# Optimization experiments

Measured on AMD Instinct MI355X. Metric: run time of the kernel, lower is better.

## Reference

```python
import jax, jax.numpy as jnp
import numpy as np
from functools import partial

C = 96
D_STATE = 16
D_CONV = 4
EXPAND = 2
D_INNER = EXPAND * C
DT_RANK = (C + 15) // 16  # ceil(96/16) = 6
EPS = 1e-6


def _ln_cf(x, w, b):
    # channels_first LayerNorm over axis=1 of [B,C,D,H,W]
    u = jnp.mean(x, axis=1, keepdims=True)
    s = jnp.mean((x - u) ** 2, axis=1, keepdims=True)
    xn = (x - u) / jnp.sqrt(s + EPS)
    return w[None, :, None, None, None] * xn + b[None, :, None, None, None]


def _ln_last(x, w, b):
    u = jnp.mean(x, axis=-1, keepdims=True)
    s = jnp.mean((x - u) ** 2, axis=-1, keepdims=True)
    return (x - u) / jnp.sqrt(s + 1e-5) * w + b


def _mamba(x, Win, conv_w, conv_b, Wx, Wdt, bdt, A_log, Dp, Wout):
    # x: [B, L, C]
    B, L, _ = x.shape
    xz = jnp.einsum('blc,ec->ble', x, Win)           # [B,L,2*di]
    xin, z = xz[..., :D_INNER], xz[..., D_INNER:]
    # depthwise causal conv along L
    xt = jnp.transpose(xin, (0, 2, 1))               # [B,di,L]
    xt = jnp.pad(xt, ((0, 0), (0, 0), (D_CONV - 1, 0)))
    xc = jax.lax.conv_general_dilated(
        xt, conv_w[:, None, :], window_strides=(1,), padding='VALID',
        feature_group_count=D_INNER, dimension_numbers=('NCH', 'OIH', 'NCH'))
    xc = jax.nn.silu(xc + conv_b[None, :, None])
    xc = jnp.transpose(xc, (0, 2, 1))                # [B,L,di]
    x_dbl = jnp.einsum('bld,ed->ble', xc, Wx)        # [B,L,dt_rank+2*ds]
    dt_r = x_dbl[..., :DT_RANK]
    Bm = x_dbl[..., DT_RANK:DT_RANK + D_STATE]       # [B,L,ds]
    Cm = x_dbl[..., DT_RANK + D_STATE:]              # [B,L,ds]
    dt = jax.nn.softplus(jnp.einsum('blr,dr->bld', dt_r, Wdt) + bdt)
    A = -jnp.exp(A_log)                              # [di,ds]
    dA = jnp.exp(dt[..., None] * A)                  # [B,L,di,ds]
    dBx = (dt * xc)[..., None] * Bm[:, :, None, :]   # [B,L,di,ds]

    def comb(e1, e2):
        a1, b1 = e1
        a2, b2 = e2
        return a1 * a2, a2 * b1 + b2

    _, h = jax.lax.associative_scan(comb, (dA, dBx), axis=1)
    y = jnp.einsum('blds,bls->bld', h, Cm) + xc * Dp
    y = y * jax.nn.silu(z)
    return jnp.einsum('bld,cd->blc', y, Wout)


def setup_inputs() -> dict:
    key = jax.random.key(0)
    ks = jax.random.split(key, 16)
    g = lambda k, sh: jax.random.normal(k, sh, dtype=jnp.float32) * 0.02
    inp = {
        'x': jax.random.normal(ks[0], (2, C, 20, 20, 20), dtype=jnp.float32),
        'ln_w': jnp.ones((C,), jnp.float32), 'ln_b': jnp.zeros((C,), jnp.float32),
        'mln_w': jnp.ones((C,), jnp.float32), 'mln_b': jnp.zeros((C,), jnp.float32),
        'Win': g(ks[1], (2 * D_INNER, C)),
        'conv_w': g(ks[2], (D_INNER, D_CONV)), 'conv_b': jnp.zeros((D_INNER,), jnp.float32),
        'Wx': g(ks[3], (DT_RANK + 2 * D_STATE, D_INNER)),
        'Wdt': g(ks[4], (D_INNER, DT_RANK)), 'bdt': g(ks[5], (D_INNER,)),
        'A_log': jnp.log(jnp.broadcast_to(jnp.arange(1, D_STATE + 1, dtype=jnp.float32), (D_INNER, D_STATE))),
        'Dp': jnp.ones((D_INNER,), jnp.float32),
        'Wout': g(ks[6], (C, D_INNER)),
        'proj_w': g(ks[7], (C, 3 * C)), 'proj_b': jnp.zeros((C,), jnp.float32),
        'fc1_w': g(ks[8], (4 * C, C)), 'fc1_b': jnp.zeros((4 * C,), jnp.float32),
        'fc2_w': g(ks[9], (C, 4 * C)), 'fc2_b': jnp.zeros((C,), jnp.float32),
    }
    return inp


def reference(x, ln_w, ln_b, mln_w, mln_b, Win, conv_w, conv_b, Wx, Wdt, bdt,
              A_log, Dp, Wout, proj_w, proj_b, fc1_w, fc1_b, fc2_w, fc2_b):
    B, Cc, Dd, Hh, Ww = x.shape
    L = Dd * Hh * Ww
    x1 = _ln_cf(x, ln_w, ln_b)
    # three directional flattenings (cube, so reshape shapes match)
    outs = []
    for perm in ((0, 1, 2, 3, 4), (0, 1, 3, 4, 2), (0, 1, 4, 2, 3)):
        xp = jnp.transpose(x1, perm)                     # [B,C,a,b,c]
        xf = jnp.transpose(xp.reshape(B, Cc, L), (0, 2, 1))  # [B,L,C]
        xf = _ln_last(xf, mln_w, mln_b)
        y = _mamba(xf, Win, conv_w, conv_b, Wx, Wdt, bdt, A_log, Dp, Wout)
        outs.append(jnp.transpose(y, (0, 2, 1)).reshape(B, Cc, Dd, Hh, Ww))
    cat = jnp.concatenate(outs, axis=1)                  # [B,3C,D,H,W]
    out1 = jnp.einsum('oc,bcdhw->bodhw', proj_w, cat) + proj_b[None, :, None, None, None]
    out_res = x + out1
    h = _ln_cf(out_res, ln_w, ln_b)
    h = jnp.einsum('oc,bcdhw->bodhw', fc1_w, h) + fc1_b[None, :, None, None, None]
    h = jax.nn.gelu(h, approximate=False)
    h = jnp.einsum('oc,bcdhw->bodhw', fc2_w, h) + fc2_b[None, :, None, None, None]
    return h + out_res
```

## Files before the change

### kernel.cpp

```cpp
#include <hip/hip_runtime.h>
#include <math.h>

#define S   8000
#define BB  2
#define CC  96
#define DI  192
#define NS  16
#define RK  6
#define GG  6
#define NC  200
#define LC  40
#define ND  38

typedef __attribute__((ext_vector_type(8))) short bf16x8;
typedef __attribute__((ext_vector_type(4))) float f32x4;
typedef __attribute__((ext_vector_type(2))) float f32x2;

__device__ __forceinline__ int pos_from_l(int dir, int l) {
  if (dir == 0) return l;
  int a  = l / 400;
  int r  = l - a * 400;
  int bq = r / 20;
  int cq = r - bq * 20;
  if (dir == 1) return cq * 400 + a * 20 + bq;
  return bq * 400 + cq * 20 + a;
}

__device__ __forceinline__ float silu(float z) {
  return z / (1.f + __expf(-z));
}

__device__ __forceinline__ unsigned short f2bf(float x) {
  unsigned int u = __float_as_uint(x);
  u += 0x7FFFu + ((u >> 16) & 1u);
  return (unsigned short)(u >> 16);
}
__device__ __forceinline__ float bf2f(unsigned short h) {
  return __uint_as_float((unsigned int)h << 16);
}

__device__ __forceinline__ float pair_sum(float y) {
  return y + __int_as_float(__builtin_amdgcn_update_dpp(
      0, __float_as_int(y), 0xB1, 0xF, 0xF, true));
}
__device__ __forceinline__ float quad_sum(float x) {
  x += __int_as_float(__builtin_amdgcn_update_dpp(0, __float_as_int(x), 0xB1, 0xF, 0xF, true));
  x += __int_as_float(__builtin_amdgcn_update_dpp(0, __float_as_int(x), 0x4E, 0xF, 0xF, true));
  return x;
}

template <int ACT, bool DOUBLE, bool OUTBF16>
__global__ __launch_bounds__(256) void k_lnmfma(const float* __restrict__ Xsrc,
    const float* __restrict__ lnw, const float* __restrict__ lnb,
    const float* __restrict__ mlnw, const float* __restrict__ mlnb,
    const float* __restrict__ Bw, const float* __restrict__ bias,
    void* __restrict__ Cout, int M, int N) {
  __shared__ float Xf[64][97];
  __shared__ unsigned short Al[64][104];
  __shared__ unsigned short Bl[96][104];
  int tid = threadIdx.x;
  int m0 = blockIdx.x * 64, n0 = blockIdx.y * 96;
  int b = m0 / S, pos0 = m0 - b * S;
  for (int idx = tid; idx < 64 * 96; idx += 256) {
    int row = idx & 63, c = idx >> 6;
    Xf[row][c] = Xsrc[((size_t)b * CC + c) * S + pos0 + row];
  }
  for (int idx = tid; idx < 96 * 24; idx += 256) {
    int bn = idx / 24, kq = idx - bn * 24;
    int n = n0 + bn;
    float4 v = make_float4(0.f, 0.f, 0.f, 0.f);
    if (n < N) v = *(const float4*)&Bw[(size_t)n * 96 + kq * 4];
    unsigned short* dst = &Bl[bn][kq * 4];
    dst[0] = f2bf(v.x); dst[1] = f2bf(v.y);
    dst[2] = f2bf(v.z); dst[3] = f2bf(v.w);
  }
  __syncthreads();
  {
    int row = tid >> 2, part = tid & 3;
    const float* xr = &Xf[row][part * 24];
    float s1 = 0.f, s2 = 0.f;
#pragma unroll
    for (int i = 0; i < 24; ++i) { float v = xr[i]; s1 += v; s2 += v * v; }
    s1 = quad_sum(s1); s2 = quad_sum(s2);
    float u = s1 * (1.f / 96.f);
    float var = s2 * (1.f / 96.f) - u * u;
    float rstd = rsqrtf(var + 1e-6f);
    if (DOUBLE) {
      float t1 = 0.f, t2 = 0.f;
#pragma unroll
      for (int i = 0; i < 24; ++i) {
        int c = part * 24 + i;
        float y1 = fmaf(lnw[c], (xr[i] - u) * rstd, lnb[c]);
        t1 += y1; t2 += y1 * y1;
      }
      t1 = quad_sum(t1); t2 = quad_sum(t2);
      float u2 = t1 * (1.f / 96.f);
      float var2 = t2 * (1.f / 96.f) - u2 * u2;
      float rstd2 = rsqrtf(var2 + 1e-5f);
#pragma unroll
      for (int i = 0; i < 24; ++i) {
        int c = part * 24 + i;
        float y1 = fmaf(lnw[c], (xr[i] - u) * rstd, lnb[c]);
        Al[row][c] = f2bf(fmaf(mlnw[c], (y1 - u2) * rstd2, mlnb[c]));
      }
    } else {
#pragma unroll
      for (int i = 0; i < 24; ++i) {
        int c = part * 24 + i;
        Al[row][c] = f2bf(fmaf(lnw[c], (xr[i] - u) * rstd, lnb[c]));
      }
    }
  }
  __syncthreads();
  int wid = tid >> 6, lane = tid & 63;
  int wr = wid >> 1, wc = wid & 1;
  int l16 = lane & 15, lk = (lane >> 4) * 8;
  f32x4 acc[2][3];
#pragma unroll
  for (int i = 0; i < 2; ++i)
#pragma unroll
    for (int j = 0; j < 3; ++j) acc[i][j] = (f32x4){0.f, 0.f, 0.f, 0.f};
#pragma unroll
  for (int kc = 0; kc < 96; kc += 32) {
    bf16x8 af[2], bfr[3];
#pragma unroll
    for (int i = 0; i < 2; ++i)
      af[i] = *(const bf16x8*)&Al[wr * 32 + i * 16 + l16][kc + lk];
#pragma unroll
    for (int j = 0; j < 3; ++j)
      bfr[j] = *(const bf16x8*)&Bl[wc * 48 + j * 16 + l16][kc + lk];
#pragma unroll
    for (int i = 0; i < 2; ++i)
#pragma unroll
      for (int j = 0; j < 3; ++j)
        acc[i][j] = __builtin_amdgcn_mfma_f32_16x16x32_bf16(
            af[i], bfr[j], acc[i][j], 0, 0, 0);
  }
#pragma unroll
  for (int i = 0; i < 2; ++i) {
#pragma unroll
    for (int j = 0; j < 3; ++j) {
#pragma unroll
      for (int v = 0; v < 4; ++v) {
        int m = m0 + wr * 32 + i * 16 + (lane >> 4) * 4 + v;
        int n = n0 + wc * 48 + j * 16 + l16;
        if (n < N) {
          float val = acc[i][j][v];
          val += bias ? bias[n] : 0.f;
          if (ACT == 1) val = 0.5f * val * (1.f + erff(val * 0.70710678118654752f));
          if (OUTBF16) ((unsigned short*)Cout)[(size_t)m * N + n] = f2bf(val);
          else         ((float*)Cout)[(size_t)m * N + n] = val;
        }
      }
    }
  }
}

#define BKP 40
template <int ACT, bool BIAS, bool RESID, bool OUT_BCS, bool GATEA, bool ABF16>
__global__ __launch_bounds__(256) void k_mfma(const void* __restrict__ Ap,
    const float* __restrict__ Bw, const float* __restrict__ bias,
    const float* __restrict__ resid, const float* __restrict__ XZg,
    float* __restrict__ Cmat, int M, int N, int K) {
  __shared__ unsigned short Al[64][BKP];
  __shared__ unsigned short Bl[96][BKP];
  int tid = threadIdx.x;
  int m0 = blockIdx.x * 64, n0 = blockIdx.y * 96;
  int wid = tid >> 6, lane = tid & 63;
  int wr = wid >> 1, wc = wid & 1;
  int l16 = lane & 15, lk = (lane >> 4) * 8;
  f32x4 acc[2][3];
#pragma unroll
  for (int i = 0; i < 2; ++i)
#pragma unroll
    for (int j = 0; j < 3; ++j) acc[i][j] = (f32x4){0.f, 0.f, 0.f, 0.f};

  for (int kk = 0; kk < K; kk += 32) {
    if (ABF16) {
      int row = tid >> 2, kq = tid & 3;
      int m = m0 + row;
      const unsigned short* As = (const unsigned short*)Ap;
      uint4 v = *(const uint4*)&As[(size_t)m * K + kk + kq * 8];
      if (GATEA) {
        unsigned short* pv = (unsigned short*)&v;
        int bb = m / S, ll = m - bb * S;
        int j = kk + kq * 8;
        int dir = j / DI; int e0 = j - dir * DI;
        int p = pos_from_l(dir, ll);
        const float4 z1 = *(const float4*)&XZg[((size_t)bb * S + p) * 384 + DI + e0];
        const float4 z2 = *(const float4*)&XZg[((size_t)bb * S + p) * 384 + DI + e0 + 4];
        pv[0] = f2bf(bf2f(pv[0]) * silu(z1.x));
        pv[1] = f2bf(bf2f(pv[1]) * silu(z1.y));
        pv[2] = f2bf(bf2f(pv[2]) * silu(z1.z));
        pv[3] = f2bf(bf2f(pv[3]) * silu(z1.w));
        pv[4] = f2bf(bf2f(pv[4]) * silu(z2.x));
        pv[5] = f2bf(bf2f(pv[5]) * silu(z2.y));
        pv[6] = f2bf(bf2f(pv[6]) * silu(z2.z));
        pv[7] = f2bf(bf2f(pv[7]) * silu(z2.w));
      }
      *(uint4*)&Al[row][kq * 8] = v;
    } else {
#pragma unroll
      for (int i = 0; i < 2; ++i) {
        int idx = tid + i * 256;
        int row = idx >> 3, kq = idx & 7;
        int m = m0 + row;
        const float* Af = (const float*)Ap;
        float4 v = *(const float4*)&Af[(size_t)m * K + kk + kq * 4];
        unsigned short* dst = &Al[row][kq * 4];
        dst[0] = f2bf(v.x); dst[1] = f2bf(v.y);
        dst[2] = f2bf(v.z); dst[3] = f2bf(v.w);
      }
    }
#pragma unroll
    for (int i = 0; i < 3; ++i) {
      int idx = tid + i * 256;
      int bn = idx >> 3, kq = idx & 7;
      int n = n0 + bn;
      float4 v = make_float4(0.f, 0.f, 0.f, 0.f);
      if (n < N) v = *(const float4*)&Bw[(size_t)n * K + kk + kq * 4];
      unsigned short* dst = &Bl[bn][kq * 4];
      dst[0] = f2bf(v.x); dst[1] = f2bf(v.y);
      dst[2] = f2bf(v.z); dst[3] = f2bf(v.w);
    }
    __syncthreads();
    bf16x8 af[2], bfr[3];
#pragma unroll
    for (int i = 0; i < 2; ++i)
      af[i] = *(const bf16x8*)&Al[wr * 32 + i * 16 + l16][lk];
#pragma unroll
    for (int j = 0; j < 3; ++j)
      bfr[j] = *(const bf16x8*)&Bl[wc * 48 + j * 16 + l16][lk];
#pragma unroll
    for (int i = 0; i < 2; ++i)
#pragma unroll
      for (int j = 0; j < 3; ++j)
        acc[i][j] = __builtin_amdgcn_mfma_f32_16x16x32_bf16(
            af[i], bfr[j], acc[i][j], 0, 0, 0);
    __syncthreads();
  }
#pragma unroll
  for (int i = 0; i < 2; ++i) {
#pragma unroll
    for (int j = 0; j < 3; ++j) {
#pragma unroll
      for (int v = 0; v < 4; ++v) {
        int m = m0 + wr * 32 + i * 16 + (lane >> 4) * 4 + v;
        int n = n0 + wc * 48 + j * 16 + l16;
        if (n < N) {
          float val = acc[i][j][v];
          if (BIAS) val += bias[n];
          if (ACT == 1) val = 0.5f * val * (1.f + erff(val * 0.70710678118654752f));
          if (RESID || OUT_BCS) {
            int bb = m / S, pp = m - bb * S;
            size_t oidx = ((size_t)bb * CC + n) * S + pp;
            if (RESID) val += resid[oidx];
            if (OUT_BCS) { Cmat[oidx] = val; continue; }
          }
          Cmat[(size_t)m * N + n] = val;
        }
      }
    }
  }
}

__global__ __launch_bounds__(256) void k_conv(const float* __restrict__ XZ,
    const float* __restrict__ cw, const float* __restrict__ cb,
    float* __restrict__ xc) {
  int t = blockIdx.x * blockDim.x + threadIdx.x;
  if (t >= GG * S * 48) return;
  int q = t % 48; int gl = t / 48; int l = gl % S; int g = gl / S;
  int e0 = q * 4;
  int b = g / 3, dir = g - (g / 3) * 3;
  float cwv[4][4];
#pragma unroll
  for (int i = 0; i < 4; ++i)
    *(float4*)cwv[i] = *(const float4*)&cw[(e0 + i) * 4];
  float4 acc = *(const float4*)&cb[e0];
#pragma unroll
  for (int k = 0; k < 4; ++k) {
    int ls = l + k - 3;
    if (ls >= 0) {
      int p = pos_from_l(dir, ls);
      const float4 xz = *(const float4*)&XZ[((size_t)b * S + p) * 384 + e0];
      acc.x = fmaf(cwv[0][k], xz.x, acc.x);
      acc.y = fmaf(cwv[1][k], xz.y, acc.y);
      acc.z = fmaf(cwv[2][k], xz.z, acc.z);
      acc.w = fmaf(cwv[3][k], xz.w, acc.w);
    }
  }
  acc.x *= 1.f / (1.f + __expf(-acc.x));
  acc.y *= 1.f / (1.f + __expf(-acc.y));
  acc.z *= 1.f / (1.f + __expf(-acc.z));
  acc.w *= 1.f / (1.f + __expf(-acc.w));
  *(float4*)&xc[(size_t)gl * DI + e0] = acc;
}

__device__ __forceinline__ void stage_bc(float (*sBC)[40],
    const float* __restrict__ xdbl, int g, int c, int tid) {
  const float* src = xdbl + ((size_t)g * S + c * LC) * ND;
  for (int i = tid; i < LC * ND; i += 192) {
    int row = i / ND, col = i - row * ND;
    int dst = (col < RK) ? col : col + 2;
    sBC[row][dst] = src[(size_t)row * ND + col];
  }
}

#define DT_COMMON(l)                                                     \
  float a = bde;                                                         \
  {                                                                      \
    float4 r0 = *(const float4*)&sBC[l][0];                              \
    float2 r1 = *(const float2*)&sBC[l][4];                              \
    a = fmaf(wdt[0], r0.x, a); a = fmaf(wdt[1], r0.y, a);                \
    a = fmaf(wdt[2], r0.z, a); a = fmaf(wdt[3], r0.w, a);                \
    a = fmaf(wdt[4], r1.x, a); a = fmaf(wdt[5], r1.y, a);                \
  }                                                                      \
  float d = fmaxf(a, 0.f) + __logf(1.f + __expf(-fabsf(a)));

__global__ __launch_bounds__(192) void k_scanA(const float* __restrict__ xc,
    const float* __restrict__ xdbl, const float* __restrict__ Wdt,
    const float* __restrict__ bdt, const float* __restrict__ A_log,
    float* __restrict__ PA, float* __restrict__ EA) {
  __shared__ float sBC[LC][40];
  int c = blockIdx.x, g = blockIdx.y;
  int tid = threadIdx.x;
  int e = blockIdx.z * 96 + (tid >> 1);
  int hf = tid & 1;
  stage_bc(sBC, xdbl, g, c, tid);
  float wdt[RK];
#pragma unroll
  for (int r = 0; r < RK; ++r) wdt[r] = Wdt[e * RK + r];
  float bde = bdt[e];
  float base = -__expf(A_log[e * NS]);
  bool fast = true;
#pragma unroll
  for (int s = 1; s < NS; ++s) {
    float aes = -__expf(A_log[e * NS + s]);
    fast = fast && (fabsf(aes / base - (float)(s + 1)) < 1e-3f);
  }
  f32x2 h2[4];
#pragma unroll
  for (int k = 0; k < 4; ++k) h2[k] = (f32x2){0.f, 0.f};
  float T = 0.f;
  const float* xptr = xc + ((size_t)g * S + c * LC) * DI + e;
  __syncthreads();
  if (fast) {
    for (int l0 = 0; l0 < LC; l0 += 8) {
      float xb[8];
#pragma unroll
      for (int j = 0; j < 8; ++j) xb[j] = xptr[(size_t)(l0 + j) * DI];
#pragma unroll
      for (int j = 0; j < 8; ++j) {
        int l = l0 + j;
        DT_COMMON(l)
        T += d;
        float w = d * xb[j];
        float r = __expf(d * base);
        float r2 = r * r, r4 = r2 * r2, r8 = r4 * r4;
        float f = hf ? r8 * r : r;
        f32x2 m0 = {f, f * r};
        f32x2 r2v = {r2, r2};
        f32x2 r4v = {r4, r4};
        f32x2 m1 = m0 * r2v, m2 = m0 * r4v, m3 = m1 * r4v;
        f32x2 wv = {w, w};
        float4 Ba = *(const float4*)&sBC[l][8 + hf * 8];
        float4 Bb = *(const float4*)&sBC[l][12 + hf * 8];
        h2[0] = m0 * h2[0] + wv * (f32x2){Ba.x, Ba.y};
        h2[1] = m1 * h2[1] + wv * (f32x2){Ba.z, Ba.w};
        h2[2] = m2 * h2[2] + wv * (f32x2){Bb.x, Bb.y};
        h2[3] = m3 * h2[3] + wv * (f32x2){Bb.z, Bb.w};
      }
    }
  } else {
    float Aes[8];
#pragma unroll
    for (int k = 0; k < 8; ++k) Aes[k] = -__expf(A_log[e * NS + hf * 8 + k]);
#pragma unroll 1
    for (int l = 0; l < LC; ++l) {
      DT_COMMON(l)
      T += d;
      float w = d * xptr[(size_t)l * DI];
#pragma unroll
      for (int k = 0; k < 8; ++k) {
        float q = __expf(d * Aes[k]);
        h2[k >> 1][k & 1] = fmaf(q, h2[k >> 1][k & 1], w * sBC[l][8 + hf * 8 + k]);
      }
    }
  }
  float* pp = PA + (((size_t)g * NC + c) * DI + e) * NS + hf * 8;
  float* ep = EA + (((size_t)g * NC + c) * DI + e) * NS + hf * 8;
  float po[8];
  if (fast) {
    float r = __expf(base * T);
    float r2 = r * r, r4 = r2 * r2, r8 = r4 * r4;
    float f = hf ? r8 * r : r;
    po[0] = f; po[1] = f * r; po[2] = f * r2; po[3] = po[1] * r2;
    po[4] = f * r4; po[5] = po[1] * r4; po[6] = po[2] * r4; po[7] = po[3] * r4;
  } else {
#pragma unroll
    for (int k = 0; k < 8; ++k)
      po[k] = __expf(-__expf(A_log[e * NS + hf * 8 + k]) * T);
  }
  *(float4*)&pp[0] = make_float4(po[0], po[1], po[2], po[3]);
  *(float4*)&pp[4] = make_float4(po[4], po[5], po[6], po[7]);
  *(float4*)&ep[0] = make_float4(h2[0][0], h2[0][1], h2[1][0], h2[1][1]);
  *(float4*)&ep[4] = make_float4(h2[2][0], h2[2][1], h2[3][0], h2[3][1]);
}

__global__ __launch_bounds__(256) void k_scanB(const float* PA,
    const float* EA, float* Hin) {
  int idx = blockIdx.x * blockDim.x + threadIdx.x;
  if (idx >= GG * DI * NS) return;
  int g = idx / (DI * NS); int es = idx - g * (DI * NS);
  size_t stride = (size_t)DI * NS;
  size_t b0 = (size_t)g * NC * stride + es;
  float h = 0.f;
  for (int c0 = 0; c0 < NC; c0 += 8) {
    float p8[8], e8[8];
#pragma unroll
    for (int j = 0; j < 8; ++j) {
      size_t ix = b0 + (size_t)(c0 + j) * stride;
      p8[j] = PA[ix]; e8[j] = EA[ix];
    }
#pragma unroll
    for (int j = 0; j < 8; ++j) {
      size_t ix = b0 + (size_t)(c0 + j) * stride;
      Hin[ix] = h;
      h = fmaf(p8[j], h, e8[j]);
    }
  }
}

__global__ __launch_bounds__(192) void k_scanC(const float* __restrict__ xc,
    const float* __restrict__ xdbl, const float* __restrict__ Wdt,
    const float* __restrict__ bdt, const float* __restrict__ A_log,
    const float* __restrict__ Hin, const float* __restrict__ Dp,
    unsigned short* __restrict__ ygb) {
  __shared__ float sBC[LC][40];
  int c = blockIdx.x, g = blockIdx.y;
  int tid = threadIdx.x;
  int e = blockIdx.z * 96 + (tid >> 1);
  int hf = tid & 1;
  const float* hp = Hin + (((size_t)g * NC + c) * DI + e) * NS + hf * 8;
  float4 h0 = *(const float4*)(hp + 0);
  float4 h1v = *(const float4*)(hp + 4);
  stage_bc(sBC, xdbl, g, c, tid);
  float wdt[RK];
#pragma unroll
  for (int r = 0; r < RK; ++r) wdt[r] = Wdt[e * RK + r];
  float bde = bdt[e];
  float dpe = Dp[e];
  float base = -__expf(A_log[e * NS]);
  bool fast = true;
#pragma unroll
  for (int s = 1; s < NS; ++s) {
    float aes = -__expf(A_log[e * NS + s]);
    fast = fast && (fabsf(aes / base - (float)(s + 1)) < 1e-3f);
  }
  f32x2 h2[4] = {{h0.x, h0.y}, {h0.z, h0.w}, {h1v.x, h1v.y}, {h1v.z, h1v.w}};
  const float* xptr = xc + ((size_t)g * S + c * LC) * DI + e;
  int b = g / 3, dir = g - (g / 3) * 3;
  unsigned short* yo = ygb + ((size_t)b * S + c * LC) * 576 + dir * DI + e;
  __syncthreads();
  if (fast) {
    for (int l0 = 0; l0 < LC; l0 += 8) {
      float xb[8];
#pragma unroll
      for (int j = 0; j < 8; ++j) xb[j] = xptr[(size_t)(l0 + j) * DI];
#pragma unroll
      for (int j = 0; j < 8; ++j) {
        int l = l0 + j;
        DT_COMMON(l)
        float xv = xb[j];
        float w = d * xv;
        float r = __expf(d * base);
        float r2 = r * r, r4 = r2 * r2, r8 = r4 * r4;
        float f = hf ? r8 * r : r;
        f32x2 m0 = {f, f * r};
        f32x2 r2v = {r2, r2};
        f32x2 r4v = {r4, r4};
        f32x2 m1 = m0 * r2v, m2 = m0 * r4v, m3 = m1 * r4v;
        f32x2 wv = {w, w};
        float4 Ba = *(const float4*)&sBC[l][8 + hf * 8];
        float4 Bb = *(const float4*)&sBC[l][12 + hf * 8];
        float4 Ca = *(const float4*)&sBC[l][24 + hf * 8];
        float4 Cb = *(const float4*)&sBC[l][28 + hf * 8];
        f32x2 yacc = {hf ? 0.f : xv * dpe, 0.f};
        h2[0] = m0 * h2[0] + wv * (f32x2){Ba.x, Ba.y};
        yacc += h2[0] * (f32x2){Ca.x, Ca.y};
        h2[1] = m1 * h2[1] + wv * (f32x2){Ba.z, Ba.w};
        yacc += h2[1] * (f32x2){Ca.z, Ca.w};
        h2[2] = m2 * h2[2] + wv * (f32x2){Bb.x, Bb.y};
        yacc += h2[2] * (f32x2){Cb.x, Cb.y};
        h2[3] = m3 * h2[3] + wv * (f32x2){Bb.z, Bb.w};
        yacc += h2[3] * (f32x2){Cb.z, Cb.w};
        float ysum = pair_sum(yacc[0] + yacc[1]);
        if (!hf) yo[(size_t)l * 576] = f2bf(ysum);
      }
    }
  } else {
    float Aes[8];
#pragma unroll
    for (int k = 0; k < 8; ++k) Aes[k] = -__expf(A_log[e * NS + hf * 8 + k]);
#pragma unroll 1
    for (int l = 0; l < LC; ++l) {
      DT_COMMON(l)
      float xv = xptr[(size_t)l * DI];
      float w = d * xv;
      float y = hf ? 0.f : xv * dpe;
#pragma unroll
      for (int k = 0; k < 8; ++k) {
        float q = __expf(d * Aes[k]);
        float hk = fmaf(q, h2[k >> 1][k & 1], w * sBC[l][8 + hf * 8 + k]);
        h2[k >> 1][k & 1] = hk;
        y = fmaf(hk, sBC[l][24 + hf * 8 + k], y);
      }
      float ysum = pair_sum(y);
      if (!hf) yo[(size_t)l * 576] = f2bf(ysum);
    }
  }
}

__global__ __launch_bounds__(256) void k_foldW(const float* __restrict__ proj_w,
    const float* __restrict__ Wout, float* __restrict__ Mcat) {
  int t = blockIdx.x * blockDim.x + threadIdx.x;
  if (t >= CC * 576) return;
  int o = t / 576; int j = t - o * 576; int dir = j / DI; int e = j - dir * DI;
  float a = 0.f;
  for (int c2 = 0; c2 < CC; ++c2)
    a = fmaf(proj_w[o * 288 + dir * CC + c2], Wout[c2 * DI + e], a);
  Mcat[t] = a;
}

extern "C" void kernel_launch(void* const* d_in, const int* in_sizes, int n_in,
                              void* d_out, int out_size, void* d_ws, size_t ws_size,
                              hipStream_t stream) {
  const float* x      = (const float*)d_in[0];
  const float* ln_w   = (const float*)d_in[1];
  const float* ln_b   = (const float*)d_in[2];
  const float* mln_w  = (const float*)d_in[3];
  const float* mln_b  = (const float*)d_in[4];
  const float* Win    = (const float*)d_in[5];
  const float* conv_w = (const float*)d_in[6];
  const float* conv_b = (const float*)d_in[7];
  const float* Wx     = (const float*)d_in[8];
  const float* Wdt    = (const float*)d_in[9];
  const float* bdt    = (const float*)d_in[10];
  const float* A_log  = (const float*)d_in[11];
  const float* Dp     = (const float*)d_in[12];
  const float* Wout   = (const float*)d_in[13];
  const float* proj_w = (const float*)d_in[14];
  const float* proj_b = (const float*)d_in[15];
  const float* fc1_w  = (const float*)d_in[16];
  const float* fc1_b  = (const float*)d_in[17];
  const float* fc2_w  = (const float*)d_in[18];
  const float* fc2_b  = (const float*)d_in[19];

  float* ws = (float*)d_ws;
  size_t off = 0;
  float* ores = ws + off; off += (size_t)BB * S * CC;
  float* XZ   = ws + off; off += (size_t)BB * S * 384;
  float* xc   = ws + off; off += (size_t)GG * S * DI;
  float* xdbl = ws + off; off += (size_t)GG * S * ND;
  float* PA   = ws + off; off += (size_t)GG * NC * DI * NS;
  float* EA   = ws + off; off += (size_t)GG * NC * DI * NS;
  float* yg   = ws + off; off += (size_t)BB * S * 576;
  float* Mcat = ws + off; off += (size_t)CC * 576;
  if (ws_size < off * sizeof(float)) return;
  float* Hin  = PA;
  unsigned short* ygb = (unsigned short*)yg;
  unsigned short* h1  = (unsigned short*)XZ;

  k_lnmfma<0, true, false><<<dim3(BB * S / 64, 4), 256, 0, stream>>>(
      x, ln_w, ln_b, mln_w, mln_b, Win, nullptr, XZ, BB * S, 384);
  k_conv<<<(GG * S * 48 + 255) / 256, 256, 0, stream>>>(XZ, conv_w, conv_b, xc);
  k_mfma<0, false, false, false, false, false>
      <<<dim3(GG * S / 64, 1), 256, 0, stream>>>(
      xc, Wx, nullptr, nullptr, nullptr, xdbl, GG * S, ND, DI);
  k_scanA<<<dim3(NC, GG, 2), 192, 0, stream>>>(xc, xdbl, Wdt, bdt, A_log, PA, EA);
  k_scanB<<<(GG * DI * NS + 255) / 256, 256, 0, stream>>>(PA, EA, Hin);
  k_scanC<<<dim3(NC, GG, 2), 192, 0, stream>>>(xc, xdbl, Wdt, bdt, A_log, Hin, Dp, ygb);
  k_foldW<<<(CC * 576 + 255) / 256, 256, 0, stream>>>(proj_w, Wout, Mcat);
  k_mfma<0, true, true, true, true, true>
      <<<dim3(BB * S / 64, 1), 256, 0, stream>>>(
      ygb, Mcat, proj_b, x, XZ, ores, BB * S, CC, 576);
  k_lnmfma<1, false, true><<<dim3(BB * S / 64, 4), 256, 0, stream>>>(
      ores, ln_w, ln_b, nullptr, nullptr, fc1_w, fc1_b, h1, BB * S, 384);
  k_mfma<0, true, true, true, false, true>
      <<<dim3(BB * S / 64, 1), 256, 0, stream>>>(
      h1, fc2_w, fc2_b, ores, nullptr, (float*)d_out, BB * S, CC, 384);
}
```

Baseline: 267.9 us.

## Store conv output in bf16 and precompute dt and decay in fp16

The conv kernel now writes xc as bf16, and the x_proj GEMM reads it as bf16. A new k_dtr kernel computes softplus(dt) and exp(dt*A0) once per element into fp16 buffers, so scanA and scanC no longer recompute them. Both scans stage only the B/C columns in shared memory. The aim is to cut memory traffic and duplicated transcendental work in the two scan passes, at the cost of an extra kernel launch, an extra round trip through memory, and reduced precision for dt and the decay factor.

```diff
diff --git a/kernel.cpp b/kernel.cpp
--- a/kernel.cpp
+++ b/kernel.cpp
@@ -1,4 +1,5 @@
 #include <hip/hip_runtime.h>
+#include <hip/hip_fp16.h>
 #include <math.h>
 
 #define S   8000
@@ -266,7 +267,7 @@
 
 __global__ __launch_bounds__(256) void k_conv(const float* __restrict__ XZ,
     const float* __restrict__ cw, const float* __restrict__ cb,
-    float* __restrict__ xc) {
+    unsigned short* __restrict__ xcb) {
   int t = blockIdx.x * blockDim.x + threadIdx.x;
   if (t >= GG * S * 48) return;
   int q = t % 48; int gl = t / 48; int l = gl % S; int g = gl / S;
@@ -289,48 +290,58 @@
       acc.w = fmaf(cwv[3][k], xz.w, acc.w);
     }
   }
-  acc.x *= 1.f / (1.f + __expf(-acc.x));
-  acc.y *= 1.f / (1.f + __expf(-acc.y));
-  acc.z *= 1.f / (1.f + __expf(-acc.z));
-  acc.w *= 1.f / (1.f + __expf(-acc.w));
-  *(float4*)&xc[(size_t)gl * DI + e0] = acc;
-}
-
-__device__ __forceinline__ void stage_bc(float (*sBC)[40],
+  unsigned short o[4];
+  o[0] = f2bf(acc.x * (1.f / (1.f + __expf(-acc.x))));
+  o[1] = f2bf(acc.y * (1.f / (1.f + __expf(-acc.y))));
+  o[2] = f2bf(acc.z * (1.f / (1.f + __expf(-acc.z))));
+  o[3] = f2bf(acc.w * (1.f / (1.f + __expf(-acc.w))));
+  *(uint2*)&xcb[(size_t)gl * DI + e0] = *(uint2*)o;
+}
+
+__global__ __launch_bounds__(256) void k_dtr(const float* __restrict__ xdbl,
+    const float* __restrict__ Wdt, const float* __restrict__ bdt,
+    const float* __restrict__ A_log, __half* __restrict__ dtb,
+    __half* __restrict__ rb) {
+  int t = blockIdx.x * blockDim.x + threadIdx.x;
+  if (t >= GG * S * DI) return;
+  int e = t % DI; int row = t / DI;
+  const float* xr = xdbl + (size_t)row * ND;
+  float a = bdt[e];
+#pragma unroll
+  for (int r = 0; r < RK; ++r) a = fmaf(Wdt[e * RK + r], xr[r], a);
+  float d = fmaxf(a, 0.f) + __logf(1.f + __expf(-fabsf(a)));
+  float base = -__expf(A_log[e * NS]);
+  dtb[t] = __float2half(d);
+  rb[t] = __float2half(__expf(d * base));
+}
+
+__device__ __forceinline__ void stage_b16(float (*sB)[16],
     const float* __restrict__ xdbl, int g, int c, int tid) {
-  const float* src = xdbl + ((size_t)g * S + c * LC) * ND;
-  for (int i = tid; i < LC * ND; i += 192) {
-    int row = i / ND, col = i - row * ND;
-    int dst = (col < RK) ? col : col + 2;
-    sBC[row][dst] = src[(size_t)row * ND + col];
-  }
-}
-
-#define DT_COMMON(l)                                                     \
-  float a = bde;                                                         \
-  {                                                                      \
-    float4 r0 = *(const float4*)&sBC[l][0];                              \
-    float2 r1 = *(const float2*)&sBC[l][4];                              \
-    a = fmaf(wdt[0], r0.x, a); a = fmaf(wdt[1], r0.y, a);                \
-    a = fmaf(wdt[2], r0.z, a); a = fmaf(wdt[3], r0.w, a);                \
-    a = fmaf(wdt[4], r1.x, a); a = fmaf(wdt[5], r1.y, a);                \
-  }                                                                      \
-  float d = fmaxf(a, 0.f) + __logf(1.f + __expf(-fabsf(a)));
-
-__global__ __launch_bounds__(192) void k_scanA(const float* __restrict__ xc,
-    const float* __restrict__ xdbl, const float* __restrict__ Wdt,
-    const float* __restrict__ bdt, const float* __restrict__ A_log,
+  const float* src = xdbl + ((size_t)g * S + c * LC) * ND + RK;
+  for (int i = tid; i < LC * 16; i += 192) {
+    int row = i >> 4, col = i & 15;
+    sB[row][col] = src[(size_t)row * ND + col];
+  }
+}
+__device__ __forceinline__ void stage_bc32(float (*sBC)[32],
+    const float* __restrict__ xdbl, int g, int c, int tid) {
+  const float* src = xdbl + ((size_t)g * S + c * LC) * ND + RK;
+  for (int i = tid; i < LC * 32; i += 192) {
+    int row = i >> 5, col = i & 31;
+    sBC[row][col] = src[(size_t)row * ND + col];
+  }
+}
+
+__global__ __launch_bounds__(192) void k_scanA(const unsigned short* __restrict__ xcb,
+    const __half* __restrict__ dtb, const __half* __restrict__ rbuf,
+    const float* __restrict__ xdbl, const float* __restrict__ A_log,
     float* __restrict__ PA, float* __restrict__ EA) {
-  __shared__ float sBC[LC][40];
+  __shared__ float sB[LC][16];
   int c = blockIdx.x, g = blockIdx.y;
   int tid = threadIdx.x;
   int e = blockIdx.z * 96 + (tid >> 1);
   int hf = tid & 1;
-  stage_bc(sBC, xdbl, g, c, tid);
-  float wdt[RK];
-#pragma unroll
-  for (int r = 0; r < RK; ++r) wdt[r] = Wdt[e * RK + r];
-  float bde = bdt[e];
+  stage_b16(sB, xdbl, g, c, tid);
   float base = -__expf(A_log[e * NS]);
   bool fast = true;
 #pragma unroll
@@ -342,29 +353,36 @@
 #pragma unroll
   for (int k = 0; k < 4; ++k) h2[k] = (f32x2){0.f, 0.f};
   float T = 0.f;
-  const float* xptr = xc + ((size_t)g * S + c * LC) * DI + e;
+  size_t sbase = ((size_t)g * S + c * LC) * DI + e;
+  const unsigned short* xp = xcb + sbase;
+  const __half* dp = dtb + sbase;
+  const __half* rp = rbuf + sbase;
   __syncthreads();
   if (fast) {
     for (int l0 = 0; l0 < LC; l0 += 8) {
-      float xb[8];
-#pragma unroll
-      for (int j = 0; j < 8; ++j) xb[j] = xptr[(size_t)(l0 + j) * DI];
+      float xb[8], db[8], rv[8];
+#pragma unroll
+      for (int j = 0; j < 8; ++j) {
+        xb[j] = bf2f(xp[(size_t)(l0 + j) * DI]);
+        db[j] = __half2float(dp[(size_t)(l0 + j) * DI]);
+        rv[j] = __half2float(rp[(size_t)(l0 + j) * DI]);
+      }
 #pragma unroll
       for (int j = 0; j < 8; ++j) {
         int l = l0 + j;
-        DT_COMMON(l)
+        float d = db[j];
         T += d;
         float w = d * xb[j];
-        float r = __expf(d * base);
+        float r = rv[j];
         float r2 = r * r, r4 = r2 * r2, r8 = r4 * r4;
         float f = hf ? r8 * r : r;
         f32x2 m0 = {f, f * r};
-        f32x2 r2v = {r2, r2};
-        f32x2 r4v = {r4, r4};
-        f32x2 m1 = m0 * r2v, m2 = m0 * r4v, m3 = m1 * r4v;
+        f32x2 m1 = m0 * (f32x2){r2, r2};
+        f32x2 m2 = m0 * (f32x2){r4, r4};
+        f32x2 m3 = m1 * (f32x2){r4, r4};
         f32x2 wv = {w, w};
-        float4 Ba = *(const float4*)&sBC[l][8 + hf * 8];
-        float4 Bb = *(const float4*)&sBC[l][12 + hf * 8];
+        float4 Ba = *(const float4*)&sB[l][hf * 8];
+        float4 Bb = *(const float4*)&sB[l][hf * 8 + 4];
         h2[0] = m0 * h2[0] + wv * (f32x2){Ba.x, Ba.y};
         h2[1] = m1 * h2[1] + wv * (f32x2){Ba.z, Ba.w};
         h2[2] = m2 * h2[2] + wv * (f32x2){Bb.x, Bb.y};
@@ -377,13 +395,13 @@
     for (int k = 0; k < 8; ++k) Aes[k] = -__expf(A_log[e * NS + hf * 8 + k]);
 #pragma unroll 1
     for (int l = 0; l < LC; ++l) {
-      DT_COMMON(l)
+      float d = __half2float(dp[(size_t)l * DI]);
       T += d;
-      float w = d * xptr[(size_t)l * DI];
+      float w = d * bf2f(xp[(size_t)l * DI]);
 #pragma unroll
       for (int k = 0; k < 8; ++k) {
         float q = __expf(d * Aes[k]);
-        h2[k >> 1][k & 1] = fmaf(q, h2[k >> 1][k & 1], w * sBC[l][8 + hf * 8 + k]);
+        h2[k >> 1][k & 1] = fmaf(q, h2[k >> 1][k & 1], w * sB[l][hf * 8 + k]);
       }
     }
   }
@@ -431,12 +449,12 @@
   }
 }
 
-__global__ __launch_bounds__(192) void k_scanC(const float* __restrict__ xc,
-    const float* __restrict__ xdbl, const float* __restrict__ Wdt,
-    const float* __restrict__ bdt, const float* __restrict__ A_log,
+__global__ __launch_bounds__(192) void k_scanC(const unsigned short* __restrict__ xcb,
+    const __half* __restrict__ dtb, const __half* __restrict__ rbuf,
+    const float* __restrict__ xdbl, const float* __restrict__ A_log,
     const float* __restrict__ Hin, const float* __restrict__ Dp,
     unsigned short* __restrict__ ygb) {
-  __shared__ float sBC[LC][40];
+  __shared__ float sBC[LC][32];
   int c = blockIdx.x, g = blockIdx.y;
   int tid = threadIdx.x;
   int e = blockIdx.z * 96 + (tid >> 1);
@@ -444,11 +462,7 @@
   const float* hp = Hin + (((size_t)g * NC + c) * DI + e) * NS + hf * 8;
   float4 h0 = *(const float4*)(hp + 0);
   float4 h1v = *(const float4*)(hp + 4);
-  stage_bc(sBC, xdbl, g, c, tid);
-  float wdt[RK];
-#pragma unroll
-  for (int r = 0; r < RK; ++r) wdt[r] = Wdt[e * RK + r];
-  float bde = bdt[e];
+  stage_bc32(sBC, xdbl, g, c, tid);
   float dpe = Dp[e];
   float base = -__expf(A_log[e * NS]);
   bool fast = true;
@@ -458,33 +472,40 @@
     fast = fast && (fabsf(aes / base - (float)(s + 1)) < 1e-3f);
   }
   f32x2 h2[4] = {{h0.x, h0.y}, {h0.z, h0.w}, {h1v.x, h1v.y}, {h1v.z, h1v.w}};
-  const float* xptr = xc + ((size_t)g * S + c * LC) * DI + e;
+  size_t sbase = ((size_t)g * S + c * LC) * DI + e;
+  const unsigned short* xp = xcb + sbase;
+  const __half* dp = dtb + sbase;
+  const __half* rp = rbuf + sbase;
   int b = g / 3, dir = g - (g / 3) * 3;
   unsigned short* yo = ygb + ((size_t)b * S + c * LC) * 576 + dir * DI + e;
   __syncthreads();
   if (fast) {
     for (int l0 = 0; l0 < LC; l0 += 8) {
-      float xb[8];
-#pragma unroll
-      for (int j = 0; j < 8; ++j) xb[j] = xptr[(size_t)(l0 + j) * DI];
+      float xb[8], db[8], rv[8];
+#pragma unroll
+      for (int j = 0; j < 8; ++j) {
+        xb[j] = bf2f(xp[(size_t)(l0 + j) * DI]);
+        db[j] = __half2float(dp[(size_t)(l0 + j) * DI]);
+        rv[j] = __half2float(rp[(size_t)(l0 + j) * DI]);
+      }
 #pragma unroll
       for (int j = 0; j < 8; ++j) {
         int l = l0 + j;
-        DT_COMMON(l)
+        float d = db[j];
         float xv = xb[j];
         float w = d * xv;
-        float r = __expf(d * base);
+        float r = rv[j];
         float r2 = r * r, r4 = r2 * r2, r8 = r4 * r4;
         float f = hf ? r8 * r : r;
         f32x2 m0 = {f, f * r};
-        f32x2 r2v = {r2, r2};
-        f32x2 r4v = {r4, r4};
-        f32x2 m1 = m0 * r2v, m2 = m0 * r4v, m3 = m1 * r4v;
+        f32x2 m1 = m0 * (f32x2){r2, r2};
+        f32x2 m2 = m0 * (f32x2){r4, r4};
+        f32x2 m3 = m1 * (f32x2){r4, r4};
         f32x2 wv = {w, w};
-        float4 Ba = *(const float4*)&sBC[l][8 + hf * 8];
-        float4 Bb = *(const float4*)&sBC[l][12 + hf * 8];
-        float4 Ca = *(const float4*)&sBC[l][24 + hf * 8];
-        float4 Cb = *(const float4*)&sBC[l][28 + hf * 8];
+        float4 Ba = *(const float4*)&sBC[l][hf * 8];
+        float4 Bb = *(const float4*)&sBC[l][hf * 8 + 4];
+        float4 Ca = *(const float4*)&sBC[l][16 + hf * 8];
+        float4 Cb = *(const float4*)&sBC[l][16 + hf * 8 + 4];
         f32x2 yacc = {hf ? 0.f : xv * dpe, 0.f};
         h2[0] = m0 * h2[0] + wv * (f32x2){Ba.x, Ba.y};
         yacc += h2[0] * (f32x2){Ca.x, Ca.y};
@@ -504,16 +525,16 @@
     for (int k = 0; k < 8; ++k) Aes[k] = -__expf(A_log[e * NS + hf * 8 + k]);
 #pragma unroll 1
     for (int l = 0; l < LC; ++l) {
-      DT_COMMON(l)
-      float xv = xptr[(size_t)l * DI];
+      float d = __half2float(dp[(size_t)l * DI]);
+      float xv = bf2f(xp[(size_t)l * DI]);
       float w = d * xv;
       float y = hf ? 0.f : xv * dpe;
 #pragma unroll
       for (int k = 0; k < 8; ++k) {
         float q = __expf(d * Aes[k]);
-        float hk = fmaf(q, h2[k >> 1][k & 1], w * sBC[l][8 + hf * 8 + k]);
+        float hk = fmaf(q, h2[k >> 1][k & 1], w * sBC[l][hf * 8 + k]);
         h2[k >> 1][k & 1] = hk;
-        y = fmaf(hk, sBC[l][24 + hf * 8 + k], y);
+        y = fmaf(hk, sBC[l][16 + hf * 8 + k], y);
       }
       float ysum = pair_sum(y);
       if (!hf) yo[(size_t)l * 576] = f2bf(ysum);
@@ -560,26 +581,35 @@
   size_t off = 0;
   float* ores = ws + off; off += (size_t)BB * S * CC;
   float* XZ   = ws + off; off += (size_t)BB * S * 384;
-  float* xc   = ws + off; off += (size_t)GG * S * DI;
+  float* xcf  = ws + off; off += (size_t)GG * S * DI / 2;
   float* xdbl = ws + off; off += (size_t)GG * S * ND;
+  float* dtf  = ws + off; off += (size_t)GG * S * DI / 2;
+  float* rf   = ws + off; off += (size_t)GG * S * DI / 2;
   float* PA   = ws + off; off += (size_t)GG * NC * DI * NS;
   float* EA   = ws + off; off += (size_t)GG * NC * DI * NS;
-  float* yg   = ws + off; off += (size_t)BB * S * 576;
+  float* yg   = ws + off; off += (size_t)BB * S * 576 / 2;
   float* Mcat = ws + off; off += (size_t)CC * 576;
   if (ws_size < off * sizeof(float)) return;
   float* Hin  = PA;
+  unsigned short* xcb = (unsigned short*)xcf;
+  __half* dtb = (__half*)dtf;
+  __half* rb  = (__half*)rf;
   unsigned short* ygb = (unsigned short*)yg;
   unsigned short* h1  = (unsigned short*)XZ;
 
   k_lnmfma<0, true, false><<<dim3(BB * S / 64, 4), 256, 0, stream>>>(
       x, ln_w, ln_b, mln_w, mln_b, Win, nullptr, XZ, BB * S, 384);
-  k_conv<<<(GG * S * 48 + 255) / 256, 256, 0, stream>>>(XZ, conv_w, conv_b, xc);
-  k_mfma<0, false, false, false, false, false>
+  k_conv<<<(GG * S * 48 + 255) / 256, 256, 0, stream>>>(XZ, conv_w, conv_b, xcb);
+  k_mfma<0, false, false, false, false, true>
       <<<dim3(GG * S / 64, 1), 256, 0, stream>>>(
-      xc, Wx, nullptr, nullptr, nullptr, xdbl, GG * S, ND, DI);
-  k_scanA<<<dim3(NC, GG, 2), 192, 0, stream>>>(xc, xdbl, Wdt, bdt, A_log, PA, EA);
+      xcb, Wx, nullptr, nullptr, nullptr, xdbl, GG * S, ND, DI);
+  k_dtr<<<(GG * S * DI + 255) / 256, 256, 0, stream>>>(
+      xdbl, Wdt, bdt, A_log, dtb, rb);
+  k_scanA<<<dim3(NC, GG, 2), 192, 0, stream>>>(
+      xcb, dtb, rb, xdbl, A_log, PA, EA);
   k_scanB<<<(GG * DI * NS + 255) / 256, 256, 0, stream>>>(PA, EA, Hin);
-  k_scanC<<<dim3(NC, GG, 2), 192, 0, stream>>>(xc, xdbl, Wdt, bdt, A_log, Hin, Dp, ygb);
+  k_scanC<<<dim3(NC, GG, 2), 192, 0, stream>>>(
+      xcb, dtb, rb, xdbl, A_log, Hin, Dp, ygb);
   k_foldW<<<(CC * 576 + 255) / 256, 256, 0, stream>>>(proj_w, Wout, Mcat);
   k_mfma<0, true, true, true, true, true>
       <<<dim3(BB * S / 64, 1), 256, 0, stream>>>(
```

After: 276.9 us. 3.4% more time.
